# Kernel optimization log

Measured on AMD Instinct MI355X. Metric: run time of the kernel, lower is better.

The kernel has to match this reference:

```python
import jax, jax.numpy as jnp
import numpy as np

BS = 2; D = 256; NH = 8; NL = 4; NP = 4; WS = 7; DFF = 1024
SHAPES = [(92, 92), (46, 46), (23, 23), (12, 12)]
LEN = sum(h * w for h, w in SHAPES)  # 11253
DH = D // NH


def _layer_norm(x, g, b):
    mu = jnp.mean(x, -1, keepdims=True)
    var = jnp.var(x, -1, keepdims=True)
    return (x - mu) * jax.lax.rsqrt(var + 1e-5) * g + b


def _bilinear(v_l, loc, H_, W_):
    # v_l: (N, nh, H_*W_, d); loc: (N, Lq, nh, P, 2) normalized in [0,1] (x, y)
    N, Lq, nh, P, _ = loc.shape
    x = loc[..., 0] * W_ - 0.5  # grid_sample align_corners=False convention
    y = loc[..., 1] * H_ - 0.5
    x0f = jnp.floor(x); y0f = jnp.floor(y)
    tx = (x - x0f).transpose(0, 2, 1, 3)  # (N, nh, Lq, P)
    ty = (y - y0f).transpose(0, 2, 1, 3)
    x0 = x0f.astype(jnp.int32).transpose(0, 2, 1, 3)
    y0 = y0f.astype(jnp.int32).transpose(0, 2, 1, 3)

    def g(yi, xi):
        valid = ((xi >= 0) & (xi < W_) & (yi >= 0) & (yi < H_)).astype(v_l.dtype)
        idx = (jnp.clip(yi, 0, H_ - 1) * W_ + jnp.clip(xi, 0, W_ - 1)).reshape(N, nh, Lq * P)
        out = jnp.take_along_axis(v_l, idx[..., None], axis=2).reshape(N, nh, Lq, P, -1)
        return out * valid[..., None]

    return (g(y0, x0) * ((1 - tx) * (1 - ty))[..., None]
            + g(y0, x0 + 1) * (tx * (1 - ty))[..., None]
            + g(y0 + 1, x0) * ((1 - tx) * ty)[..., None]
            + g(y0 + 1, x0 + 1) * (tx * ty)[..., None])


def setup_inputs() -> dict:
    key = jax.random.key(0)
    ks = jax.random.split(key, 20)
    s = 0.02
    inp = {}
    inp['src'] = jax.random.normal(ks[0], (BS, LEN, D), jnp.float32)
    inp['pos'] = jax.random.normal(ks[1], (BS, LEN, D), jnp.float32)
    inp['reference_points'] = jax.random.uniform(ks[2], (BS, LEN, NL, 2), jnp.float32)
    c = WS // 2
    ys, xs = jnp.meshgrid(jnp.arange(WS) - c, jnp.arange(WS) - c, indexing='ij')
    inp['window_grid'] = jnp.stack([xs, ys], -1).reshape(WS * WS, 2).astype(jnp.float32)
    for l, (h, w) in enumerate(SHAPES):
        inp[f'mask{l}'] = jax.random.normal(ks[3 + l], (BS, 1, h, w), jnp.float32)
    inp['spatial_shapes'] = jnp.array(SHAPES, jnp.int32)
    starts = np.cumsum([0] + [h * w for h, w in SHAPES])[:NL]
    inp['level_start_index'] = jnp.array(starts, jnp.int32)
    # parse_mask: Conv2d(1, n_heads, 1) per level -> per-head scale + bias
    inp['pm_w'] = jax.random.normal(ks[7], (NL, NH), jnp.float32) * s
    inp['pm_b'] = jax.random.normal(ks[8], (NL, NH), jnp.float32) * s
    inp['Wv'] = jax.random.normal(ks[9], (D, D), jnp.float32) * s
    inp['bv'] = jnp.zeros((D,), jnp.float32)
    inp['Wo'] = jax.random.normal(ks[10], (D, D), jnp.float32) * s
    inp['bo'] = jnp.zeros((D,), jnp.float32)
    inp['ln1_g'] = jnp.ones((D,), jnp.float32)
    inp['ln1_b'] = jnp.zeros((D,), jnp.float32)
    inp['W1'] = jax.random.normal(ks[11], (D, DFF), jnp.float32) * s
    inp['b1'] = jnp.zeros((DFF,), jnp.float32)
    inp['W2'] = jax.random.normal(ks[12], (DFF, D), jnp.float32) * s
    inp['b2'] = jnp.zeros((D,), jnp.float32)
    inp['ln2_g'] = jnp.ones((D,), jnp.float32)
    inp['ln2_b'] = jnp.zeros((D,), jnp.float32)
    return inp


def reference(src, pos, reference_points, window_grid, mask0, mask1, mask2, mask3,
              spatial_shapes, level_start_index, pm_w, pm_b, Wv, bv, Wo, bo,
              ln1_g, ln1_b, W1, b1, W2, b2, ln2_g, ln2_b):
    masks = [mask0, mask1, mask2, mask3]
    p = WS // 2
    offs, samp = [], []
    for l, (H_, W_) in enumerate(SHAPES):
        # 1x1 conv from 1 -> NH channels
        m = masks[l] * pm_w[l][None, :, None, None] + pm_b[l][None, :, None, None]  # (BS,NH,H,W)
        mp = jnp.pad(m, ((0, 0), (0, 0), (p, p), (p, p)))
        # unfold: (BS, NH, WS*WS, H*W), kernel positions row-major
        patches = jnp.stack([mp[:, :, i:i + H_, j:j + W_] for i in range(WS) for j in range(WS)], axis=2)
        patches = patches.reshape(BS, NH, WS * WS, H_ * W_).transpose(0, 1, 3, 2)  # (BS,NH,HW,WS^2)
        vals, idx = jax.lax.top_k(patches, NP)  # (BS,NH,HW,NP)
        off = window_grid[idx]  # (BS,NH,HW,NP,2)
        offs.append(off.transpose(0, 2, 1, 3, 4))   # (BS,HW,NH,NP,2)
        samp.append(vals.transpose(0, 2, 1, 3))     # (BS,HW,NH,NP)
    offsets = jnp.concatenate(offs, axis=1)       # (BS,LEN,NH,NP,2)
    pred_sampled = jnp.concatenate(samp, axis=1)  # (BS,LEN,NH,NP)

    # MSDeformAttn (encoder mode: external offsets + mask-derived attention logits)
    value = (src @ Wv + bv).reshape(BS, LEN, NH, DH)
    attn = jax.nn.softmax(
        jnp.broadcast_to(pred_sampled[:, :, :, None, :], (BS, LEN, NH, NL, NP)).reshape(BS, LEN, NH, NL * NP),
        axis=-1).reshape(BS, LEN, NH, NL, NP)
    norm = jnp.array([[w, h] for h, w in SHAPES], jnp.float32)  # (NL, 2) as (W, H)
    loc = reference_points[:, :, None, :, None, :] + offsets[:, :, :, None, :, :] / norm[None, None, None, :, None, :]

    out = jnp.zeros((BS, LEN, NH, DH), src.dtype)
    s0 = 0
    for l, (H_, W_) in enumerate(SHAPES):
        v_l = value[:, s0:s0 + H_ * W_].transpose(0, 2, 1, 3)  # (BS,NH,HW,DH)
        sampled = _bilinear(v_l, loc[:, :, :, l], H_, W_)       # (BS,NH,LEN,NP,DH)
        out = out + jnp.einsum('nhqpd,nqhp->nqhd', sampled, attn[:, :, :, l])
        s0 += H_ * W_
    attn_out = out.reshape(BS, LEN, D) @ Wo + bo

    x = _layer_norm(src + attn_out, ln1_g, ln1_b)
    x2 = jax.nn.relu(x @ W1 + b1) @ W2 + b2
    return _layer_norm(x + x2, ln2_g, ln2_b)
```

## Files before the change

### kernel.cpp

```cpp
#include <hip/hip_runtime.h>
#include <cstddef>
#include <cstdint>

#define LEN_T 11253
#define TOK   22506
#define NHEADS 8
#define DMODEL 256

#define SBAR() __builtin_amdgcn_sched_barrier(0)
#define WVM(n) asm volatile("s_waitcnt vmcnt(" #n ")" ::: "memory")

typedef __attribute__((ext_vector_type(8))) short short8;
typedef __attribute__((ext_vector_type(4))) float f32x4;

__device__ __forceinline__ unsigned short f2bf(float f) {
  union { float f; unsigned u; } v; v.f = f;
  unsigned r = v.u + 0x7fffu + ((v.u >> 16) & 1u);
  return (unsigned short)(r >> 16);
}
__device__ __forceinline__ float bfhi2f(unsigned u) {
  union { unsigned u; float f; } v; v.u = u & 0xffff0000u; return v.f;
}
__device__ __forceinline__ float bflo2f(unsigned u) {
  union { unsigned u; float f; } v; v.u = u << 16; return v.f;
}
__device__ __forceinline__ float bf2f(unsigned short s) {
  union { unsigned u; float f; } v; v.u = (unsigned)s << 16; return v.f;
}
__device__ __forceinline__ void gld_lds16(const void* g, void* l) {
  __builtin_amdgcn_global_load_lds(
      (const __attribute__((address_space(1))) void*)g,
      (__attribute__((address_space(3))) void*)l, 16, 0, 0);
}

__device__ __forceinline__ void ins4(float v, int ji,
    float& t0, float& t1, float& t2, float& t3,
    int& i0, int& i1, int& i2, int& i3)
{
  bool a0 = v > t0, a1 = v > t1, a2 = v > t2, a3 = v > t3;
  t3 = a3 ? (a2 ? t2 : v) : t3;  i3 = a3 ? (a2 ? i2 : ji) : i3;
  t2 = a2 ? (a1 ? t1 : v) : t2;  i2 = a2 ? (a1 ? i1 : ji) : i2;
  t1 = a1 ? (a0 ? t0 : v) : t1;  i1 = a1 ? (a0 ? i0 : ji) : i1;
  t0 = a0 ? v : t0;              i0 = a0 ? ji : i0;
}

__global__ __launch_bounds__(256) void pre_kernel(
    const float* __restrict__ src, unsigned short* __restrict__ src_bf,
    const float* __restrict__ m0, const float* __restrict__ m1,
    const float* __restrict__ m2, const float* __restrict__ m3,
    const float* __restrict__ pm_w, const float* __restrict__ pm_b,
    const float* __restrict__ Wv, const float* __restrict__ Wo,
    const float* __restrict__ W1, const float* __restrict__ W2,
    unsigned short* __restrict__ Wv_t, unsigned short* __restrict__ Wo_t,
    unsigned short* __restrict__ W1_t, unsigned short* __restrict__ W2_t,
    unsigned* __restrict__ offp, float* __restrict__ attw)
{
  int blk = blockIdx.x;
  if (blk >= 1344) {
    int i = (blk - 1344) * 2048 + threadIdx.x * 8;
    if (i < TOK * DMODEL) {
      float4 a = *(const float4*)(src + i);
      float4 b = *(const float4*)(src + i + 4);
      uint4 o;
      o.x = (unsigned)f2bf(a.x) | ((unsigned)f2bf(a.y) << 16);
      o.y = (unsigned)f2bf(a.z) | ((unsigned)f2bf(a.w) << 16);
      o.z = (unsigned)f2bf(b.x) | ((unsigned)f2bf(b.y) << 16);
      o.w = (unsigned)f2bf(b.z) | ((unsigned)f2bf(b.w) << 16);
      *(uint4*)(src_bf + i) = o;
    }
    return;
  }
  if (blk >= 704) {
    int cb = blk - 704;
    const float* W; unsigned short* Bt; int lk, ln, base;
    if (cb < 64)       { W = Wv; Bt = Wv_t; lk = 8;  ln = 8;  base = cb; }
    else if (cb < 128) { W = Wo; Bt = Wo_t; lk = 8;  ln = 8;  base = cb - 64; }
    else if (cb < 384) { W = W1; Bt = W1_t; lk = 8;  ln = 10; base = cb - 128; }
    else               { W = W2; Bt = W2_t; lk = 10; ln = 8;  base = cb - 384; }
    int i4 = (base * 256 + threadIdx.x) * 4;
    int n  = i4 >> lk;
    int k  = i4 & ((1 << lk) - 1);
    ushort4 o;
    o.x = f2bf(W[((size_t)(k + 0) << ln) + n]);
    o.y = f2bf(W[((size_t)(k + 1) << ln) + n]);
    o.z = f2bf(W[((size_t)(k + 2) << ln) + n]);
    o.w = f2bf(W[((size_t)(k + 3) << ln) + n]);
    *(ushort4*)(Bt + i4) = o;
    return;
  }
  int t = blk * 256 + threadIdx.x;
  if (t >= TOK * NHEADS) return;
  int h  = t & 7;
  int bq = t >> 3;
  int b  = bq / LEN_T;
  int q  = bq - b * LEN_T;
  int l, H_, W_;
  const float* mk;
  if (q < 8464)       { l = 0; H_ = 92; W_ = 92; mk = m0; }
  else if (q < 10580) { l = 1; H_ = 46; W_ = 46; mk = m1; }
  else if (q < 11109) { l = 2; H_ = 23; W_ = 23; mk = m2; }
  else                { l = 3; H_ = 12; W_ = 12; mk = m3; }
  int st = (l == 0) ? 0 : (l == 1) ? 8464 : (l == 2) ? 10580 : 11109;
  int pos = q - st;
  int rr = pos / W_;
  int cc = pos - rr * W_;
  float w  = pm_w[l * NHEADS + h];
  float bb = pm_b[l * NHEADS + h];
  const float* mp = mk + (size_t)b * H_ * W_;

  float t0=-1e30f,t1=-1e30f,t2=-1e30f,t3=-1e30f;
  int   i0=0,i1=0,i2=0,i3=0;
  for (int i = 0; i < 7; ++i) {
    int yy = rr + i - 3;
    #pragma unroll
    for (int j = 0; j < 7; ++j) {
      int xx = cc + j - 3;
      float v = 0.f;
      if (yy >= 0 && yy < H_ && xx >= 0 && xx < W_)
        v = mp[(size_t)yy * W_ + xx] * w + bb;
      ins4(v, j | (i << 4), t0, t1, t2, t3, i0, i1, i2, i3);
    }
  }
  float e1 = __expf(t1 - t0);
  float e2 = __expf(t2 - t0);
  float e3 = __expf(t3 - t0);
  float inv = 1.f / (4.f * (1.f + e1 + e2 + e3));
  float4 wout; wout.x = inv; wout.y = e1 * inv; wout.z = e2 * inv; wout.w = e3 * inv;
  *(float4*)(attw + (size_t)t * 4) = wout;
  offp[t] = (unsigned)i0 | ((unsigned)i1 << 8)
          | ((unsigned)i2 << 16) | ((unsigned)i3 << 24);
}

__global__ __launch_bounds__(256) void sample_kernel(
    const unsigned short* __restrict__ Vb, const float* __restrict__ refpts,
    const unsigned* __restrict__ offp, const float* __restrict__ attw,
    unsigned short* __restrict__ outp)
{
  __shared__ int4  sidx[4][128];
  __shared__ float4 swgt[4][128];
  const int wv   = threadIdx.x >> 6;
  const int lane = threadIdx.x & 63;
  const int bx = blockIdx.x & 7, by = blockIdx.x >> 3;
  const int nb = bx * 703 + min(bx, 3) + by;
  const int blk = nb * 4 + wv;
  const bool ok = blk < TOK;

  if (ok) {
    const int b = (blk >= LEN_T) ? 1 : 0;
    const float* rp = refpts + (size_t)blk * 8;
    #pragma unroll
    for (int e = 0; e < 2; ++e) {
      int t = lane * 2 + e;
      int h = t & 7, lp = t >> 3;
      int l = lp >> 2, p = lp & 3;
      unsigned pb = (offp[(size_t)blk * 8 + h] >> (8 * p)) & 0xffu;
      float ox = (float)(int)(pb & 15u) - 3.f;
      float oy = (float)(int)(pb >> 4)  - 3.f;
      float aw = attw[((size_t)blk * 8 + h) * 4 + p];
      int H_ = (l == 0) ? 92 : (l == 1) ? 46 : (l == 2) ? 23 : 12;
      int st = (l == 0) ? 0  : (l == 1) ? 8464 : (l == 2) ? 10580 : 11109;
      float xx = rp[2 * l]     * (float)H_ - 0.5f + ox;
      float yy = rp[2 * l + 1] * (float)H_ - 0.5f + oy;
      float x0f = floorf(xx), y0f = floorf(yy);
      float tx = xx - x0f, ty = yy - y0f;
      int x0 = (int)x0f, y0 = (int)y0f;
      int base = b * LEN_T + st;
      float wc[4] = {(1.f - tx) * (1.f - ty), tx * (1.f - ty),
                     (1.f - tx) * ty,         tx * ty};
      int4 idx; float4 wg;
      int xs[4] = {x0, x0 + 1, x0, x0 + 1};
      int ys[4] = {y0, y0, y0 + 1, y0 + 1};
      int   id[4]; float wgt[4];
      #pragma unroll
      for (int c = 0; c < 4; ++c) {
        int xi = xs[c], yi = ys[c];
        bool v_ = (xi >= 0) & (xi < H_) & (yi >= 0) & (yi < H_);
        id[c]  = base + min(max(yi, 0), H_ - 1) * H_ + min(max(xi, 0), H_ - 1);
        wgt[c] = v_ ? aw * wc[c] : 0.f;
      }
      idx.x = id[0]; idx.y = id[1]; idx.z = id[2]; idx.w = id[3];
      wg.x = wgt[0]; wg.y = wgt[1]; wg.z = wgt[2]; wg.w = wgt[3];
      sidx[wv][t] = idx;
      swgt[wv][t] = wg;
    }
  }
  __syncthreads();

  if (ok) {
    const int h = lane >> 3, dg = lane & 7;
    const unsigned short* vb = Vb + h * 32 + dg * 4;
    f32x4 acc = {0.f, 0.f, 0.f, 0.f};

    uint2  u[2][8];
    float4 wg[2][2];

    #pragma unroll
    for (int j = 0; j < 2; ++j) {
      int4 idx  = sidx[wv][j * 8 + h];
      wg[0][j]  = swgt[wv][j * 8 + h];
      u[0][j*4+0] = *(const uint2*)(vb + (size_t)idx.x * DMODEL);
      u[0][j*4+1] = *(const uint2*)(vb + (size_t)idx.y * DMODEL);
      u[0][j*4+2] = *(const uint2*)(vb + (size_t)idx.z * DMODEL);
      u[0][j*4+3] = *(const uint2*)(vb + (size_t)idx.w * DMODEL);
    }
    SBAR();
    #pragma unroll
    for (int bt = 0; bt < 8; ++bt) {
      const int cur = bt & 1, nxt = cur ^ 1;
      if (bt < 7) {
        #pragma unroll
        for (int j = 0; j < 2; ++j) {
          int lp = (bt + 1) * 2 + j;
          int4 idx   = sidx[wv][lp * 8 + h];
          wg[nxt][j] = swgt[wv][lp * 8 + h];
          u[nxt][j*4+0] = *(const uint2*)(vb + (size_t)idx.x * DMODEL);
          u[nxt][j*4+1] = *(const uint2*)(vb + (size_t)idx.y * DMODEL);
          u[nxt][j*4+2] = *(const uint2*)(vb + (size_t)idx.z * DMODEL);
          u[nxt][j*4+3] = *(const uint2*)(vb + (size_t)idx.w * DMODEL);
        }
      }
      SBAR();
      #pragma unroll
      for (int j = 0; j < 2; ++j) {
        const float4 w4 = wg[cur][j];
        const uint2 u0 = u[cur][j*4+0], u1 = u[cur][j*4+1];
        const uint2 u2 = u[cur][j*4+2], u3 = u[cur][j*4+3];
        acc.x += w4.x * bflo2f(u0.x) + w4.y * bflo2f(u1.x) + w4.z * bflo2f(u2.x) + w4.w * bflo2f(u3.x);
        acc.y += w4.x * bfhi2f(u0.x) + w4.y * bfhi2f(u1.x) + w4.z * bfhi2f(u2.x) + w4.w * bfhi2f(u3.x);
        acc.z += w4.x * bflo2f(u0.y) + w4.y * bflo2f(u1.y) + w4.z * bflo2f(u2.y) + w4.w * bflo2f(u3.y);
        acc.w += w4.x * bfhi2f(u0.y) + w4.y * bfhi2f(u1.y) + w4.z * bfhi2f(u2.y) + w4.w * bfhi2f(u3.y);
      }
    }
    uint2 o;
    o.x = (unsigned)f2bf(acc.x) | ((unsigned)f2bf(acc.y) << 16);
    o.y = (unsigned)f2bf(acc.z) | ((unsigned)f2bf(acc.w) << 16);
    *(uint2*)(outp + (size_t)blk * DMODEL + h * 32 + dg * 4) = o;
  }
}

template<int EPI, int KC>
__global__ __launch_bounds__(256, 2) void gemm_pw(
    const short* __restrict__ Ab, const short* __restrict__ Bt,
    const float* __restrict__ bias, const float* __restrict__ res,
    const unsigned short* __restrict__ resb,
    const float* __restrict__ lng, const float* __restrict__ lnb,
    float* __restrict__ C, unsigned short* __restrict__ Cb,
    int M, int N)
{
  constexpr int K  = KC * 256;
  constexpr int NK = KC * 8;
  __shared__ short ring[4][3][3072] __attribute__((aligned(16)));
  __shared__ float2 lnred[32][4];
  const int tid  = threadIdx.x;
  const int w    = tid >> 6;
  const int lane = tid & 63;
  const int row0  = blockIdx.x * 32;
  const int ncol0 = blockIdx.y * 256;
  const int wn0   = ncol0 + w * 64;
  const int colq = lane & 15, quad = lane >> 4;

  f32x4 acc[2][4];
  #pragma unroll
  for (int i = 0; i < 2; ++i)
    #pragma unroll
    for (int j = 0; j < 4; ++j) acc[i][j] = (f32x4){0.f, 0.f, 0.f, 0.f};

  const int lr = lane >> 2, ls = lane & 3;
  const int gs8 = ((ls ^ ((lr + (lr >> 2)) & 3)) << 3);
  const int ar0 = min(row0 + lr,      M - 1);
  const int ar1 = min(row0 + 16 + lr, M - 1);
  const int br  = wn0 + lr;

  auto stage = [&](int kb, int slot) {
    short* dst = &ring[w][slot][0];
    const int kg = kb * 32 + gs8;
    gld_lds16(Ab + (size_t)ar0 * K + kg, dst + lane * 8);
    gld_lds16(Ab + (size_t)ar1 * K + kg, dst + 512 + lane * 8);
    #pragma unroll
    for (int r = 0; r < 4; ++r)
      gld_lds16(Bt + (size_t)(br + 16 * r) * K + kg,
                dst + 1024 + r * 512 + lane * 8);
  };

  const int rdo = ((quad ^ ((colq + (colq >> 2)) & 3)) << 3);

  SBAR();
  stage(0, 0);
  stage(1, 1);
  for (int kb = 0; kb < NK; ++kb) {
    if (kb + 2 < NK) stage(kb + 2, (kb + 2) % 3);
    if (kb < NK - 2)       WVM(12);
    else if (kb == NK - 2) WVM(6);
    else                   WVM(0);
    const short* cur = &ring[w][kb % 3][0];
    short8 af[2], bf[4];
    #pragma unroll
    for (int mt = 0; mt < 2; ++mt)
      af[mt] = *(const short8*)(cur + (mt * 16 + colq) * 32 + rdo);
    #pragma unroll
    for (int nt = 0; nt < 4; ++nt)
      bf[nt] = *(const short8*)(cur + 1024 + (nt * 16 + colq) * 32 + rdo);
    #pragma unroll
    for (int mt = 0; mt < 2; ++mt)
      #pragma unroll
      for (int nt = 0; nt < 4; ++nt)
        acc[mt][nt] = __builtin_amdgcn_mfma_f32_16x16x32_bf16(
            af[mt], bf[nt], acc[mt][nt], 0, 0, 0);
    SBAR();
  }
  SBAR();

  float bia[4];
  #pragma unroll
  for (int nt = 0; nt < 4; ++nt) bia[nt] = bias[wn0 + nt * 16 + colq];

  if constexpr (EPI == 1 || EPI == 3) {
    #pragma unroll
    for (int mt = 0; mt < 2; ++mt) {
      #pragma unroll
      for (int r = 0; r < 4; ++r) {
        int lrow = mt * 16 + quad * 4 + r;
        int rowc = min(row0 + lrow, M - 1);
        float s = 0.f, sq = 0.f;
        #pragma unroll
        for (int nt = 0; nt < 4; ++nt) {
          float rv;
          if constexpr (EPI == 1)
            rv = res[(size_t)rowc * 256 + wn0 + nt * 16 + colq];
          else
            rv = bf2f(resb[(size_t)rowc * 256 + wn0 + nt * 16 + colq]);
          float f = acc[mt][nt][r] + bia[nt] + rv;
          acc[mt][nt][r] = f;
          s += f; sq += f * f;
        }
        #pragma unroll
        for (int off = 1; off < 16; off <<= 1) {
          s  += __shfl_xor(s,  off, 64);
          sq += __shfl_xor(sq, off, 64);
        }
        if (colq == 0) lnred[lrow][w] = (float2){s, sq};
      }
    }
    __syncthreads();
    #pragma unroll
    for (int mt = 0; mt < 2; ++mt) {
      #pragma unroll
      for (int r = 0; r < 4; ++r) {
        int lrow = mt * 16 + quad * 4 + r;
        int row  = row0 + lrow;
        if (row >= M) continue;
        float2 p0 = lnred[lrow][0], p1 = lnred[lrow][1];
        float2 p2 = lnred[lrow][2], p3 = lnred[lrow][3];
        float mu  = (p0.x + p1.x + p2.x + p3.x) * (1.f / 256.f);
        float var = (p0.y + p1.y + p2.y + p3.y) * (1.f / 256.f) - mu * mu;
        float rs  = rsqrtf(var + 1e-5f);
        #pragma unroll
        for (int nt = 0; nt < 4; ++nt) {
          int col = wn0 + nt * 16 + colq;
          float o = (acc[mt][nt][r] - mu) * rs * lng[col] + lnb[col];
          if constexpr (EPI == 1)
            Cb[(size_t)row * 256 + col] = f2bf(o);
          else
            C[(size_t)row * 256 + col] = o;
        }
      }
    }
  } else {
    #pragma unroll
    for (int mt = 0; mt < 2; ++mt) {
      #pragma unroll
      for (int r = 0; r < 4; ++r) {
        int row = row0 + mt * 16 + quad * 4 + r;
        if (row < M) {
          #pragma unroll
          for (int nt = 0; nt < 4; ++nt) {
            float f = acc[mt][nt][r] + bia[nt];
            if constexpr (EPI == 2) f = fmaxf(f, 0.f);
            Cb[(size_t)row * N + wn0 + nt * 16 + colq] = f2bf(f);
          }
        }
      }
    }
  }
}

extern "C" void kernel_launch(void* const* d_in, const int* in_sizes, int n_in,
                              void* d_out, int out_size, void* d_ws, size_t ws_size,
                              hipStream_t stream)
{
  const float* src    = (const float*)d_in[0];
  const float* refpts = (const float*)d_in[2];
  const float* m0   = (const float*)d_in[4];
  const float* m1   = (const float*)d_in[5];
  const float* m2   = (const float*)d_in[6];
  const float* m3   = (const float*)d_in[7];
  const float* pm_w = (const float*)d_in[10];
  const float* pm_b = (const float*)d_in[11];
  const float* Wv   = (const float*)d_in[12];
  const float* bv   = (const float*)d_in[13];
  const float* Wo   = (const float*)d_in[14];
  const float* bo   = (const float*)d_in[15];
  const float* ln1g = (const float*)d_in[16];
  const float* ln1b = (const float*)d_in[17];
  const float* W1   = (const float*)d_in[18];
  const float* b1   = (const float*)d_in[19];
  const float* W2   = (const float*)d_in[20];
  const float* b2   = (const float*)d_in[21];
  const float* ln2g = (const float*)d_in[22];
  const float* ln2b = (const float*)d_in[23];
  float* out = (float*)d_out;
  char*  w   = (char*)d_ws;

  unsigned short* Vb      = (unsigned short*)(w);
  unsigned short* attnpre = (unsigned short*)(w + 11523072);
  unsigned short* h1      = (unsigned short*)(w + 23046144);
  char*           tail    = w + 69138432;
  float*          attw    = (float*)(tail);
  unsigned*       offp    = (unsigned*)(tail + 2880768);
  unsigned short* Wv_t    = (unsigned short*)(tail + 3600960);
  unsigned short* Wo_t    = (unsigned short*)(tail + 3732032);
  unsigned short* W1_t    = (unsigned short*)(tail + 3863104);
  unsigned short* W2_t    = (unsigned short*)(tail + 4387392);
  unsigned short* x_bf    = attnpre;
  unsigned short* src_bf  = h1;

  pre_kernel<<<dim3(4160), 256, 0, stream>>>(
      src, src_bf, m0, m1, m2, m3, pm_w, pm_b, Wv, Wo, W1, W2,
      Wv_t, Wo_t, W1_t, W2_t, offp, attw);

  gemm_pw<0, 1><<<dim3(704, 1), 256, 0, stream>>>(
      (const short*)src_bf, (const short*)Wv_t, bv, nullptr, nullptr,
      nullptr, nullptr, nullptr, Vb, TOK, 256);

  sample_kernel<<<dim3(5627), 256, 0, stream>>>(
      Vb, refpts, offp, attw, attnpre);

  gemm_pw<1, 1><<<dim3(704, 1), 256, 0, stream>>>(
      (const short*)attnpre, (const short*)Wo_t, bo, src, nullptr,
      ln1g, ln1b, nullptr, x_bf, TOK, 256);

  gemm_pw<2, 1><<<dim3(704, 4), 256, 0, stream>>>(
      (const short*)x_bf, (const short*)W1_t, b1, nullptr, nullptr,
      nullptr, nullptr, nullptr, h1, TOK, 1024);

  gemm_pw<3, 4><<<dim3(704, 1), 256, 0, stream>>>(
      (const short*)h1, (const short*)W2_t, b2, nullptr, x_bf,
      ln2g, ln2b, out, nullptr, TOK, 256);
}
```

Measured before the change: 310.6 us.

## Stage full A tile in LDS once and stream B fragments directly into registers

Replaces the per-wave triple-buffered LDS ring (A and B staged per k-step with manual vmcnt waits) with a single upfront load of the block's full 32xK A tile into swizzled shared memory. Weight fragments for B are instead read straight from global memory into registers and double-buffered across k-steps. This removes redundant per-wave A staging and the LDS round trip for B, but the K=1024 GEMM now uses 64KB of LDS per block, which can limit occupancy. The main loop is also fully unrolled, which raises register pressure.

```diff
diff --git a/kernel.cpp b/kernel.cpp
--- a/kernel.cpp
+++ b/kernel.cpp
@@ -8,7 +8,6 @@
 #define DMODEL 256
 
 #define SBAR() __builtin_amdgcn_sched_barrier(0)
-#define WVM(n) asm volatile("s_waitcnt vmcnt(" #n ")" ::: "memory")
 
 typedef __attribute__((ext_vector_type(8))) short short8;
 typedef __attribute__((ext_vector_type(4))) float f32x4;
@@ -238,8 +237,8 @@
   }
 }
 
-template<int EPI, int KC>
-__global__ __launch_bounds__(256, 2) void gemm_pw(
+template<int EPI, int LOG2K>
+__global__ __launch_bounds__(256, 2) void gemm_v6(
     const short* __restrict__ Ab, const short* __restrict__ Bt,
     const float* __restrict__ bias, const float* __restrict__ res,
     const unsigned short* __restrict__ resb,
@@ -247,16 +246,14 @@
     float* __restrict__ C, unsigned short* __restrict__ Cb,
     int M, int N)
 {
-  constexpr int K  = KC * 256;
-  constexpr int NK = KC * 8;
-  __shared__ short ring[4][3][3072] __attribute__((aligned(16)));
+  constexpr int K  = 1 << LOG2K;
+  constexpr int NK = K / 32;
+  constexpr int NI = K / 64;
+  __shared__ short As[32 * K] __attribute__((aligned(16)));
   __shared__ float2 lnred[32][4];
-  const int tid  = threadIdx.x;
-  const int w    = tid >> 6;
-  const int lane = tid & 63;
-  const int row0  = blockIdx.x * 32;
-  const int ncol0 = blockIdx.y * 256;
-  const int wn0   = ncol0 + w * 64;
+  const int tid = threadIdx.x, w = tid >> 6, lane = tid & 63;
+  const int row0 = blockIdx.x * 32;
+  const int wn0  = blockIdx.y * 256 + w * 64;
   const int colq = lane & 15, quad = lane >> 4;
 
   f32x4 acc[2][4];
@@ -265,50 +262,46 @@
     #pragma unroll
     for (int j = 0; j < 4; ++j) acc[i][j] = (f32x4){0.f, 0.f, 0.f, 0.f};
 
-  const int lr = lane >> 2, ls = lane & 3;
-  const int gs8 = ((ls ^ ((lr + (lr >> 2)) & 3)) << 3);
-  const int ar0 = min(row0 + lr,      M - 1);
-  const int ar1 = min(row0 + 16 + lr, M - 1);
-  const int br  = wn0 + lr;
-
-  auto stage = [&](int kb, int slot) {
-    short* dst = &ring[w][slot][0];
-    const int kg = kb * 32 + gs8;
-    gld_lds16(Ab + (size_t)ar0 * K + kg, dst + lane * 8);
-    gld_lds16(Ab + (size_t)ar1 * K + kg, dst + 512 + lane * 8);
-    #pragma unroll
-    for (int r = 0; r < 4; ++r)
-      gld_lds16(Bt + (size_t)(br + 16 * r) * K + kg,
-                dst + 1024 + r * 512 + lane * 8);
+  {
+    const size_t gb = (size_t)row0 << LOG2K;
+    #pragma unroll
+    for (int i = 0; i < NI; ++i) {
+      int o   = w * (8 << LOG2K) + i * 512 + lane * 8;
+      int r   = o >> LOG2K;
+      int src = (o & ~31) | (((((o >> 3) & 3) ^ (r & 3)) & 3) << 3);
+      gld_lds16(Ab + gb + src, As + o);
+    }
+  }
+
+  short8 bqA[4], bqB[4];
+  auto loadB = [&](int kb, short8* dst) {
+    #pragma unroll
+    for (int nt = 0; nt < 4; ++nt)
+      dst[nt] = *(const short8*)(Bt + ((size_t)(wn0 + nt * 16 + colq) << LOG2K)
+                                    + kb * 32 + quad * 8);
   };
-
-  const int rdo = ((quad ^ ((colq + (colq >> 2)) & 3)) << 3);
-
-  SBAR();
-  stage(0, 0);
-  stage(1, 1);
+  loadB(0, bqA);
+  __syncthreads();
+
+  #pragma unroll
   for (int kb = 0; kb < NK; ++kb) {
-    if (kb + 2 < NK) stage(kb + 2, (kb + 2) % 3);
-    if (kb < NK - 2)       WVM(12);
-    else if (kb == NK - 2) WVM(6);
-    else                   WVM(0);
-    const short* cur = &ring[w][kb % 3][0];
-    short8 af[2], bf[4];
-    #pragma unroll
-    for (int mt = 0; mt < 2; ++mt)
-      af[mt] = *(const short8*)(cur + (mt * 16 + colq) * 32 + rdo);
-    #pragma unroll
-    for (int nt = 0; nt < 4; ++nt)
-      bf[nt] = *(const short8*)(cur + 1024 + (nt * 16 + colq) * 32 + rdo);
+    short8* cur = (kb & 1) ? bqB : bqA;
+    short8* nxt = (kb & 1) ? bqA : bqB;
+    if (kb + 1 < NK) loadB(kb + 1, nxt);
+    short8 af[2];
+    #pragma unroll
+    for (int mt = 0; mt < 2; ++mt) {
+      int r = mt * 16 + colq;
+      af[mt] = *(const short8*)(As + ((size_t)r << LOG2K) + kb * 32
+                                + ((quad ^ (r & 3)) << 3));
+    }
     #pragma unroll
     for (int mt = 0; mt < 2; ++mt)
       #pragma unroll
       for (int nt = 0; nt < 4; ++nt)
         acc[mt][nt] = __builtin_amdgcn_mfma_f32_16x16x32_bf16(
-            af[mt], bf[nt], acc[mt][nt], 0, 0, 0);
-    SBAR();
-  }
-  SBAR();
+            af[mt], cur[nt], acc[mt][nt], 0, 0, 0);
+  }
 
   float bia[4];
   #pragma unroll
@@ -428,22 +421,22 @@
       src, src_bf, m0, m1, m2, m3, pm_w, pm_b, Wv, Wo, W1, W2,
       Wv_t, Wo_t, W1_t, W2_t, offp, attw);
 
-  gemm_pw<0, 1><<<dim3(704, 1), 256, 0, stream>>>(
+  gemm_v6<0, 8><<<dim3(704, 1), 256, 0, stream>>>(
       (const short*)src_bf, (const short*)Wv_t, bv, nullptr, nullptr,
       nullptr, nullptr, nullptr, Vb, TOK, 256);
 
   sample_kernel<<<dim3(5627), 256, 0, stream>>>(
       Vb, refpts, offp, attw, attnpre);
 
-  gemm_pw<1, 1><<<dim3(704, 1), 256, 0, stream>>>(
+  gemm_v6<1, 8><<<dim3(704, 1), 256, 0, stream>>>(
       (const short*)attnpre, (const short*)Wo_t, bo, src, nullptr,
       ln1g, ln1b, nullptr, x_bf, TOK, 256);
 
-  gemm_pw<2, 1><<<dim3(704, 4), 256, 0, stream>>>(
+  gemm_v6<2, 8><<<dim3(704, 4), 256, 0, stream>>>(
       (const short*)x_bf, (const short*)W1_t, b1, nullptr, nullptr,
       nullptr, nullptr, nullptr, h1, TOK, 1024);
 
-  gemm_pw<3, 4><<<dim3(704, 1), 256, 0, stream>>>(
+  gemm_v6<3, 10><<<dim3(704, 1), 256, 0, stream>>>(
       (const short*)h1, (const short*)W2_t, b2, nullptr, x_bf,
       ln2g, ln2b, out, nullptr, TOK, 256);
 }
```

Result: slower. 334.5 us (+7.7%).
